# Kernel optimization log

Measured on AMD Instinct MI355X. Metric: run time of the kernel, lower is better.

The kernel has to match this reference:

```python
import jax, jax.numpy as jnp
import numpy as np
from jax import lax

B, NE, ZD, GAMMA, BETA = 16384, 512, 32, 0.99, 1.0

def conv2d(x, w, b, stride, pad):
    y = lax.conv_general_dilated(x, w, (stride, stride), [(pad, pad), (pad, pad)],
                                 dimension_numbers=('NCHW', 'OIHW', 'NCHW'))
    return y if b is None else y + b[None, :, None, None]

def convt2d(x, w, b, stride, pad):
    # torch ConvTranspose2d(w: [in,out,kh,kw]) == dilated conv with flipped, transposed kernel
    k = w.shape[2]
    wf = jnp.flip(w, (2, 3)).transpose(1, 0, 2, 3)  # -> [out,in,kh,kw]
    p = k - 1 - pad
    y = lax.conv_general_dilated(x, wf, (1, 1), [(p, p), (p, p)], lhs_dilation=(stride, stride),
                                 dimension_numbers=('NCHW', 'OIHW', 'NCHW'))
    return y + b[None, :, None, None]

def res_stack(x, w1, w2):
    # ResidualLayer: relu -> conv3x3 (32->64) -> relu -> conv1x1 (64->32), add; stack ends with relu
    r = jax.nn.relu(x)
    r = conv2d(r, w1, None, 1, 1)
    r = jax.nn.relu(r)
    r = conv2d(r, w2, None, 1, 0)
    return jax.nn.relu(x + r)

def linear(x, w, b):
    return x @ w.T + b

def setup_inputs() -> dict:
    key = jax.random.key(0)
    ks = jax.random.split(key, 24)
    g = lambda k, s, sc=0.05: (jax.random.normal(k, s) * sc).astype(jnp.float32)
    inp = {
        'x': jax.random.uniform(ks[0], (B, 1, 28, 28), dtype=jnp.float32),
        'conv1_w': g(ks[1], (16, 1, 4, 4)), 'conv1_b': jnp.zeros((16,), jnp.float32),
        'conv2_w': g(ks[2], (32, 16, 4, 4)), 'conv2_b': jnp.zeros((32,), jnp.float32),
        'res1_w1': g(ks[3], (64, 32, 3, 3)), 'res1_w2': g(ks[4], (32, 64, 1, 1)),
        'fc1_w': g(ks[5], (224, 1568)), 'fc1_b': jnp.zeros((224,), jnp.float32),
        'fc2_w': g(ks[6], (ZD, 224)), 'fc2_b': jnp.zeros((ZD,), jnp.float32),
        'emb': jax.random.uniform(ks[7], (NE, ZD), jnp.float32, -1.0 / NE, 1.0 / NE),
        'n_mat': jnp.ones((NE,), jnp.float32),
        'm_mat': jnp.ones((NE, ZD), jnp.float32),
        'fc3_w': g(ks[8], (224, ZD)), 'fc3_b': jnp.zeros((224,), jnp.float32),
        'fc4_w': g(ks[9], (1568, 224)), 'fc4_b': jnp.zeros((1568,), jnp.float32),
        'res2_w1': g(ks[10], (64, 32, 3, 3)), 'res2_w2': g(ks[11], (32, 64, 1, 1)),
        'convt1_w': g(ks[12], (32, 16, 4, 4)), 'convt1_b': jnp.zeros((16,), jnp.float32),
        'convt2_w': g(ks[13], (16, 1, 4, 4)), 'convt2_b': jnp.zeros((1,), jnp.float32),
    }
    return inp

def vq(z, emb, n_mat, m_mat):
    # z: [N, ZD]; nearest-codeword assignment
    d = (jnp.sum(z * z, 1, keepdims=True) + jnp.sum(emb * emb, 1)
         - 2.0 * (z @ emb.T))                                   # [N, NE]
    idx = jnp.argmin(d, axis=1)                                  # [N]
    z_q = jnp.take(emb, idx, axis=0)                             # [N, ZD]
    counts = jax.ops.segment_sum(jnp.ones((z.shape[0],), z.dtype), idx, num_segments=NE)
    sums = jax.ops.segment_sum(lax.stop_gradient(z), idx, num_segments=NE)
    n_new = n_mat * GAMMA + counts * (1.0 - GAMMA)
    m_new = m_mat * GAMMA + sums * (1.0 - GAMMA)
    emb_new = m_new / n_new[:, None]
    commit_loss = BETA * jnp.mean((lax.stop_gradient(z_q) - z) ** 2)
    quant_loss = jnp.mean((z_q - lax.stop_gradient(z)) ** 2)
    z_q_st = z + lax.stop_gradient(z_q - z)                      # straight-through
    e_mean = counts / z.shape[0]
    perplexity = jnp.exp(-jnp.sum(e_mean * jnp.log(e_mean + 1e-10)))
    return quant_loss, commit_loss, z_q_st, perplexity, emb_new

def reference(x, conv1_w, conv1_b, conv2_w, conv2_b, res1_w1, res1_w2,
              fc1_w, fc1_b, fc2_w, fc2_b, emb, n_mat, m_mat,
              fc3_w, fc3_b, fc4_w, fc4_b, res2_w1, res2_w2,
              convt1_w, convt1_b, convt2_w, convt2_b):
    # encoder: 28x28 -> 14x14 -> 7x7
    h = jax.nn.relu(conv2d(x, conv1_w, conv1_b, 2, 1))
    h = conv2d(h, conv2_w, conv2_b, 2, 1)
    h = res_stack(h, res1_w1, res1_w2)
    h = h.reshape(h.shape[0], -1)                                # [B, 1568]
    h = jax.nn.relu(linear(h, fc1_w, fc1_b))
    z = linear(h, fc2_w, fc2_b)                                  # [B, ZD]
    quant_loss, commit_loss, z_q, perplexity, emb_new = vq(z, emb, n_mat, m_mat)
    # decoder
    h = jax.nn.relu(linear(z_q, fc3_w, fc3_b))
    h = jax.nn.relu(linear(h, fc4_w, fc4_b))
    h = h.reshape(-1, 32, 7, 7)
    h = res_stack(h, res2_w1, res2_w2)
    h = jax.nn.relu(convt2d(h, convt1_w, convt1_b, 2, 1))
    x_rec = convt2d(h, convt2_w, convt2_b, 2, 1)                 # [B,1,28,28]
    return x_rec, quant_loss, commit_loss, perplexity, emb_new
```

## Files before the change

### kernel.cpp

```cpp
#include <hip/hip_runtime.h>
#include <math.h>

#define NB 16384
typedef unsigned short ushort_t;
typedef unsigned int uint_t;
typedef __attribute__((ext_vector_type(8))) short short8;
typedef __attribute__((ext_vector_type(4))) float fx4;

static const size_t OFF_HB    = 0;
static const size_t OFF_F1B   = 12845056;
static const size_t OFF_F3B   = 14680064;
static const size_t OFF_Z     = 16515072;
static const size_t OFF_IDX   = 17039360;
static const size_t OFF_ZQB   = 17055744;
static const size_t OFF_CNT   = 17317888;
static const size_t OFF_SUM   = 17318400;
static const size_t OFF_LOSS  = 17334784;
static const size_t OFF_WENC  = 17334848;
static const size_t OFF_WT1B  = 17343040;
static const size_t OFF_WR1B  = 17351232;
static const size_t OFF_WR2B  = 17360448;
static const size_t OFF_W2B1  = 17369664;
static const size_t OFF_W2B2  = 17370688;
static const size_t OFF_FC1WB = 17371712;
static const size_t OFF_FC2WB = 17547328;
static const size_t OFF_FC3WB = 17550912;
static const size_t OFF_FC4WB = 17554496;

static __device__ __forceinline__ ushort_t f2bf(float f) {
  union { float f; uint_t u; } v; v.f = f;
  return (ushort_t)((v.u + 0x7fffu + ((v.u >> 16) & 1u)) >> 16);
}
static __device__ __forceinline__ float bf2f(ushort_t h) {
  union { uint_t u; float f; } v; v.u = ((uint_t)h) << 16;
  return v.f;
}

__global__ __launch_bounds__(256) void k_prep(
    const float* __restrict__ c2w, const float* __restrict__ r1w1,
    const float* __restrict__ r1w2, const float* __restrict__ r2w1,
    const float* __restrict__ r2w2, const float* __restrict__ t1w,
    const float* __restrict__ fc1w, const float* __restrict__ fc2w,
    const float* __restrict__ fc3w, const float* __restrict__ fc4w,
    float* __restrict__ ws)
{
  int gid = blockIdx.x * 256 + threadIdx.x;
  if (gid == 0) ws[OFF_LOSS] = 0.f;
  if (gid >= 774144) return;
  ushort_t* wencb = (ushort_t*)(ws + OFF_WENC);
  ushort_t* wt1b  = (ushort_t*)(ws + OFF_WT1B);
  ushort_t* wr1b  = (ushort_t*)(ws + OFF_WR1B);
  ushort_t* wr2b  = (ushort_t*)(ws + OFF_WR2B);
  ushort_t* w2b1  = (ushort_t*)(ws + OFF_W2B1);
  ushort_t* w2b2  = (ushort_t*)(ws + OFF_W2B2);
  ushort_t* fc1wb = (ushort_t*)(ws + OFF_FC1WB);
  ushort_t* fc2wb = (ushort_t*)(ws + OFF_FC2WB);
  ushort_t* fc3wb = (ushort_t*)(ws + OFF_FC3WB);
  ushort_t* fc4wb = (ushort_t*)(ws + OFF_FC4WB);
  int i = gid;
  if (i < 8192) {
    int kidx = i & 31, rest = i >> 5, co = rest & 31, kb = rest >> 5;
    int ky = kb >> 1, k2 = kb & 1, kxs = kidx >> 4, ci = kidx & 15;
    wencb[i] = f2bf(c2w[co*256 + ci*16 + ky*4 + 2*k2 + kxs]);
  } else if (i < 16384) {
    int j = i - 8192, ci = j & 31, rest = j >> 5, co = rest & 15, kk = rest >> 4;
    wt1b[j] = f2bf(t1w[ci*256 + co*16 + kk]);
  } else if (i < 34816) {
    int j = i - 16384, ci = j & 31, r = j >> 5, co = r & 63, kk = r >> 6;
    wr1b[j] = f2bf(r1w1[co*288 + ci*9 + kk]);
  } else if (i < 53248) {
    int j = i - 34816, ci = j & 31, r = j >> 5, co = r & 63, kk = r >> 6;
    wr2b[j] = f2bf(r2w1[co*288 + ci*9 + kk]);
  } else if (i < 55296) {
    int j = i - 53248; w2b1[j] = f2bf(r1w2[j]);
  } else if (i < 57344) {
    int j = i - 55296; w2b2[j] = f2bf(r2w2[j]);
  } else if (i < 408576) {
    int j = i - 57344; fc1wb[j] = f2bf(fc1w[j]);
  } else if (i < 415744) {
    int j = i - 408576; fc2wb[j] = f2bf(fc2w[j]);
  } else if (i < 422912) {
    int j = i - 415744; fc3wb[j] = f2bf(fc3w[j]);
  } else {
    int j = i - 422912; fc4wb[j] = f2bf(fc4w[j]);
  }
}

__global__ __launch_bounds__(256) void k_enc(const float* __restrict__ x,
    const float* __restrict__ w1, const float* __restrict__ b1,
    const ushort_t* __restrict__ wencb, const float* __restrict__ b2,
    ushort_t* __restrict__ hb)
{
  __shared__ float xin[30][32];
  __shared__ ushort_t ph1b[256*24];
  __shared__ ushort_t outl[1568];
  int b = blockIdx.x, t = threadIdx.x, l = t & 63, w = t >> 6;
  int pr = l & 15, g = l >> 4;
  short8 bf[8][2];
  #pragma unroll
  for (int kb = 0; kb < 8; ++kb)
    #pragma unroll
    for (int nt = 0; nt < 2; ++nt)
      bf[kb][nt] = *(const short8*)(wencb + (size_t)(kb*32 + nt*16 + pr)*32 + g*8);
  uint_t* pz = (uint_t*)ph1b;
  for (int i = t; i < 3072; i += 256) pz[i] = 0;
  float* xp = &xin[0][0];
  for (int i = t; i < 960; i += 256) xp[i] = 0.f;
  __syncthreads();
  const float* xb = x + (size_t)b*784;
  for (int i = t; i < 784; i += 256) xin[i/28 + 1][i%28 + 1] = xb[i];
  __syncthreads();
  char* phc = (char*)ph1b;
  for (int i = t; i < 3136; i += 256) {
    int p = i >> 4, co = i & 15, oy = p/14, ox = p%14;
    float acc = b1[co];
    #pragma unroll
    for (int ky = 0; ky < 4; ++ky)
      #pragma unroll
      for (int kx = 0; kx < 4; ++kx)
        acc += xin[2*oy+ky][2*ox+kx] * w1[co*16 + ky*4 + kx];
    int prow = (oy+1)*16 + (ox+1);
    *(ushort_t*)(phc + prow*48 + co*2) = f2bf(fmaxf(acc, 0.f));
  }
  __syncthreads();
  int p = w*16 + pr; if (p > 48) p = 48;
  int oy = p/7, ox = p%7;
  fx4 acc2[2];
  acc2[0] = (fx4){0.f,0.f,0.f,0.f}; acc2[1] = (fx4){0.f,0.f,0.f,0.f};
  #pragma unroll
  for (int kb = 0; kb < 8; ++kb) {
    int ky = kb >> 1, k2 = kb & 1;
    int prow = (2*oy + ky)*16 + 2*ox + 2*k2 + (g >> 1);
    short8 afr = *(const short8*)(phc + prow*48 + (g & 1)*16);
    acc2[0] = __builtin_amdgcn_mfma_f32_16x16x32_bf16(afr, bf[kb][0], acc2[0], 0, 0, 0);
    acc2[1] = __builtin_amdgcn_mfma_f32_16x16x32_bf16(afr, bf[kb][1], acc2[1], 0, 0, 0);
  }
  #pragma unroll
  for (int nt = 0; nt < 2; ++nt) {
    int co = nt*16 + pr;
    float bv = b2[co];
    #pragma unroll
    for (int i = 0; i < 4; ++i) {
      int pix = w*16 + g*4 + i;
      if (pix < 49) outl[co*49 + pix] = f2bf(acc2[nt][i] + bv);
    }
  }
  __syncthreads();
  uint_t* dst = (uint_t*)(hb + (size_t)b*1568);
  const uint_t* so = (const uint_t*)outl;
  for (int j = t; j < 784; j += 256) dst[j] = so[j];
}

__global__ __launch_bounds__(256) void k_res(ushort_t* __restrict__ hb,
    const ushort_t* __restrict__ wrb, const ushort_t* __restrict__ w2b)
{
  __shared__ ushort_t pinT[3456];
  __shared__ ushort_t rl[4096];
  __shared__ ushort_t hrawb[1568];
  __shared__ ushort_t outl[1568];
  int b = blockIdx.x, t = threadIdx.x, l = t & 63, w = t >> 6, g = l >> 4;

  short8 bfr[9];
  #pragma unroll
  for (int o = 0; o < 9; ++o)
    bfr[o] = *(const short8*)(wrb + (size_t)(o*64 + w*16 + (l & 15))*32 + g*8);

  uint_t* pz = (uint_t*)pinT;
  for (int i = t; i < 1728; i += 256) pz[i] = 0;
  __syncthreads();

  const uint_t* src = (const uint_t*)(hb + (size_t)b*1568);
  char* pinc = (char*)pinT;
  for (int j = t; j < 784; j += 256) {
    uint_t u = src[j];
    ((uint_t*)hrawb)[j] = u;
    #pragma unroll
    for (int h = 0; h < 2; ++h) {
      int i = 2*j + h;
      ushort_t us = (ushort_t)(h ? (u >> 16) : (u & 0xffff));
      ushort_t ur = (us & 0x8000) ? (ushort_t)0 : us;
      int ci = i / 49, p = i % 49, y = p / 7, xx = p % 7;
      int ppix = (y + 1)*12 + (xx + 1);
      int byte = ((ppix << 6) + (ci << 1)) ^ ((ppix & 6) << 3);
      *(ushort_t*)(pinc + byte) = ur;
    }
  }
  __syncthreads();

  fx4 acc[4];
  #pragma unroll
  for (int mt = 0; mt < 4; ++mt) acc[mt] = (fx4){0.f, 0.f, 0.f, 0.f};
  int pb[4];
  #pragma unroll
  for (int mt = 0; mt < 4; ++mt) {
    int p = mt*16 + (l & 15); if (p > 48) p = 48;
    pb[mt] = (p / 7)*12 + (p % 7);
  }
  #pragma unroll
  for (int mt = 0; mt < 4; ++mt) {
    #pragma unroll
    for (int o = 0; o < 9; ++o) {
      int ppix = pb[mt] + (o / 3)*12 + (o % 3);
      int byte = ((ppix << 6) + (g << 4)) ^ ((ppix & 6) << 3);
      short8 afr = *(const short8*)(pinc + byte);
      acc[mt] = __builtin_amdgcn_mfma_f32_16x16x32_bf16(afr, bfr[o], acc[mt], 0, 0, 0);
    }
  }
  char* rlc = (char*)rl;
  #pragma unroll
  for (int mt = 0; mt < 4; ++mt) {
    #pragma unroll
    for (int i = 0; i < 4; ++i) {
      int pixr = mt*16 + g*4 + i;
      int co2 = w*16 + (l & 15);
      int byte = ((pixr << 7) + (co2 << 1)) ^ ((pixr & 7) << 4);
      *(ushort_t*)(rlc + byte) = f2bf(fmaxf(acc[mt][i], 0.f));
    }
  }
  __syncthreads();

  fx4 a1[2];
  a1[0] = (fx4){0.f,0.f,0.f,0.f}; a1[1] = (fx4){0.f,0.f,0.f,0.f};
  int prr = w*16 + (l & 15);
  #pragma unroll
  for (int kf = 0; kf < 2; ++kf) {
    int byte = ((prr << 7) + (kf << 6) + (g << 4)) ^ ((prr & 7) << 4);
    short8 ar = *(const short8*)(rlc + byte);
    #pragma unroll
    for (int nt = 0; nt < 2; ++nt) {
      short8 br = *(const short8*)(w2b + (size_t)(nt*16 + (l & 15))*64 + kf*32 + g*8);
      a1[nt] = __builtin_amdgcn_mfma_f32_16x16x32_bf16(ar, br, a1[nt], 0, 0, 0);
    }
  }
  #pragma unroll
  for (int nt = 0; nt < 2; ++nt) {
    #pragma unroll
    for (int i = 0; i < 4; ++i) {
      int pix = w*16 + g*4 + i;
      if (pix < 49) {
        int co2 = nt*16 + (l & 15);
        int idx2 = co2*49 + pix;
        float v = bf2f(hrawb[idx2]) + a1[nt][i];
        outl[idx2] = f2bf(fmaxf(v, 0.f));
      }
    }
  }
  __syncthreads();
  uint_t* dst = (uint_t*)(hb + (size_t)b*1568);
  const uint_t* so = (const uint_t*)outl;
  for (int j = t; j < 784; j += 256) dst[j] = so[j];
}

template<int BNF, bool OUTBF16, bool RELU>
__global__ __launch_bounds__(256) void k_mm(const ushort_t* __restrict__ A,
    const ushort_t* __restrict__ Wb, const float* __restrict__ bias,
    void* __restrict__ C, int M, int N, int K)
{
  __shared__ ushort_t As[2048];
  int t = threadIdx.x, l = t & 63, w = t >> 6, g = l >> 4;
  int m0 = blockIdx.x * 64, n0 = blockIdx.y * (BNF * 16);
  fx4 acc[BNF];
  #pragma unroll
  for (int nt = 0; nt < BNF; ++nt) acc[nt] = (fx4){0.f, 0.f, 0.f, 0.f};
  char* asc = (char*)As;
  int srow = t >> 2, sks = (t & 3) * 8;
  int sbyte = ((srow << 6) + (sks << 1)) ^ ((srow & 6) << 3);
  int arow = w*16 + (l & 15);
  int abyte = ((arow << 6) + (g << 4)) ^ ((arow & 6) << 3);
  for (int k0 = 0; k0 < K; k0 += 32) {
    short8 av = *(const short8*)(A + (size_t)(m0 + srow)*K + k0 + sks);
    __syncthreads();
    *(short8*)(asc + sbyte) = av;
    __syncthreads();
    short8 afr = *(const short8*)(asc + abyte);
    #pragma unroll
    for (int nt = 0; nt < BNF; ++nt) {
      short8 bfr = *(const short8*)(Wb + (size_t)(n0 + nt*16 + (l & 15))*K + k0 + g*8);
      acc[nt] = __builtin_amdgcn_mfma_f32_16x16x32_bf16(afr, bfr, acc[nt], 0, 0, 0);
    }
  }
  #pragma unroll
  for (int nt = 0; nt < BNF; ++nt) {
    int col = n0 + nt*16 + (l & 15);
    float bv = bias[col];
    #pragma unroll
    for (int i = 0; i < 4; ++i) {
      int row = m0 + w*16 + g*4 + i;
      float v = acc[nt][i] + bv;
      if (RELU) v = fmaxf(v, 0.f);
      if (OUTBF16) ((ushort_t*)C)[(size_t)row*N + col] = f2bf(v);
      else         ((float*)C)[(size_t)row*N + col] = v;
    }
  }
}

__global__ __launch_bounds__(256) void k_vq_assign(const float* __restrict__ z,
    const float* __restrict__ emb, ushort_t* __restrict__ zqb, int* __restrict__ idx,
    float* __restrict__ loss)
{
  __shared__ float esq[512];
  int t = threadIdx.x;
  int n = blockIdx.x * 256 + t;
  for (int e = t; e < 512; e += 256) {
    const float4* ep = (const float4*)&emb[e*32];
    float s = 0.f;
    #pragma unroll
    for (int q = 0; q < 8; ++q) { float4 v = ep[q]; s += v.x*v.x + v.y*v.y + v.z*v.z + v.w*v.w; }
    esq[e] = s;
  }
  __syncthreads();
  float zv[32];
  const float4* zp = (const float4*)&z[n*32];
  float zz = 0.f;
  #pragma unroll
  for (int q = 0; q < 8; ++q) {
    float4 v = zp[q];
    zv[4*q]=v.x; zv[4*q+1]=v.y; zv[4*q+2]=v.z; zv[4*q+3]=v.w;
    zz += v.x*v.x + v.y*v.y + v.z*v.z + v.w*v.w;
  }
  float best = 3.4e38f; int bi = 0;
  for (int e = 0; e < 512; ++e) {
    const float4* ep = (const float4*)&emb[e*32];
    float dot = 0.f;
    #pragma unroll
    for (int q = 0; q < 8; ++q) {
      float4 v = ep[q];
      dot += zv[4*q]*v.x + zv[4*q+1]*v.y + zv[4*q+2]*v.z + zv[4*q+3]*v.w;
    }
    float d = zz + esq[e] - 2.f*dot;
    if (d < best) { best = d; bi = e; }
  }
  idx[n] = bi;
  const float4* bp = (const float4*)&emb[bi*32];
  uint_t* zo = (uint_t*)(zqb + (size_t)n*32);
  float ls = 0.f;
  #pragma unroll
  for (int q = 0; q < 8; ++q) {
    float4 v = bp[q];
    zo[q*2]   = (uint_t)f2bf(v.x) | ((uint_t)f2bf(v.y) << 16);
    zo[q*2+1] = (uint_t)f2bf(v.z) | ((uint_t)f2bf(v.w) << 16);
    float d0 = v.x - zv[4*q], d1 = v.y - zv[4*q+1];
    float d2 = v.z - zv[4*q+2], d3 = v.w - zv[4*q+3];
    ls += d0*d0 + d1*d1 + d2*d2 + d3*d3;
  }
  #pragma unroll
  for (int m = 32; m >= 1; m >>= 1) ls += __shfl_xor(ls, m);
  if ((t & 63) == 0) atomicAdd(loss, ls);
}

__global__ __launch_bounds__(64) void k_vq_reduce(const int* __restrict__ idx,
    const float* __restrict__ z, float* __restrict__ counts, float* __restrict__ sums)
{
  int e = blockIdx.x, t = threadIdx.x;
  float cnt = 0.f, sv[32];
  #pragma unroll
  for (int k = 0; k < 32; ++k) sv[k] = 0.f;
  for (int n = t; n < 16384; n += 64) {
    if (idx[n] == e) {
      cnt += 1.f;
      const float4* zp = (const float4*)&z[n*32];
      #pragma unroll
      for (int q = 0; q < 8; ++q) {
        float4 v = zp[q];
        sv[4*q] += v.x; sv[4*q+1] += v.y; sv[4*q+2] += v.z; sv[4*q+3] += v.w;
      }
    }
  }
  #pragma unroll
  for (int m = 32; m >= 1; m >>= 1) {
    cnt += __shfl_xor(cnt, m);
    #pragma unroll
    for (int k = 0; k < 32; ++k) sv[k] += __shfl_xor(sv[k], m);
  }
  if (t == 0) {
    counts[e] = cnt;
    #pragma unroll
    for (int k = 0; k < 32; ++k) sums[e*32 + k] = sv[k];
  }
}

__global__ __launch_bounds__(512) void k_vq_final(const float* __restrict__ counts,
    const float* __restrict__ sums, const float* __restrict__ n_mat,
    const float* __restrict__ m_mat, const float* __restrict__ loss,
    float* __restrict__ out)
{
  __shared__ float red[8];
  int t = threadIdx.x;
  float c = counts[t];
  float nn = n_mat[t]*0.99f + c*0.01f;
  #pragma unroll
  for (int k = 0; k < 32; ++k) {
    float mn = m_mat[t*32+k]*0.99f + sums[t*32+k]*0.01f;
    out[12845059 + t*32 + k] = mn / nn;
  }
  float em = c * (1.f/16384.f);
  float ht = em * logf(em + 1e-10f);
  #pragma unroll
  for (int m = 32; m >= 1; m >>= 1) ht += __shfl_xor(ht, m);
  if ((t & 63) == 0) red[t >> 6] = ht;
  __syncthreads();
  if (t == 0) {
    float H = 0.f;
    #pragma unroll
    for (int i = 0; i < 8; ++i) H += red[i];
    float q = loss[0] * (1.f/524288.f);
    out[12845056] = q;
    out[12845057] = q;
    out[12845058] = expf(-H);
  }
}

__global__ __launch_bounds__(256) void k_dec(const ushort_t* __restrict__ h5,
    const ushort_t* __restrict__ wt1b, const float* __restrict__ bt1,
    const float* __restrict__ wt2, const float* __restrict__ bt2,
    float* __restrict__ out)
{
  __shared__ ushort_t pinT[3456];
  __shared__ ushort_t pt1b[256*20];
  __shared__ float w2l[256];
  __shared__ float outl[784];
  int b = blockIdx.x, t = threadIdx.x, l = t & 63, w = t >> 6;
  int pr = l & 15, g = l >> 4;
  int py = w >> 1, px = w & 1;
  short8 bfr[4];
  #pragma unroll
  for (int r = 0; r < 2; ++r)
    #pragma unroll
    for (int c = 0; c < 2; ++c) {
      int kk = (3 - py - 2*r)*4 + (3 - px - 2*c);
      bfr[r*2 + c] = *(const short8*)(wt1b + (size_t)(kk*16 + pr)*32 + g*8);
    }
  uint_t* pz = (uint_t*)pinT;
  for (int i = t; i < 1728; i += 256) pz[i] = 0;
  uint_t* qz = (uint_t*)pt1b;
  for (int i = t; i < 2560; i += 256) qz[i] = 0;
  if (t < 256) w2l[t] = wt2[t];
  __syncthreads();
  const uint_t* src = (const uint_t*)(h5 + (size_t)b*1568);
  char* pinc = (char*)pinT;
  for (int j = t; j < 784; j += 256) {
    uint_t u = src[j];
    #pragma unroll
    for (int h = 0; h < 2; ++h) {
      int i = 2*j + h;
      ushort_t us = (ushort_t)(h ? (u >> 16) : (u & 0xffff));
      int ci = i / 49, p = i % 49, y = p / 7, xx = p % 7;
      int ppix = (y + 1)*12 + (xx + 1);
      int byte = ((ppix << 6) + (ci << 1)) ^ ((ppix & 6) << 3);
      *(ushort_t*)(pinc + byte) = us;
    }
  }
  __syncthreads();
  fx4 acc[4];
  #pragma unroll
  for (int mt = 0; mt < 4; ++mt) acc[mt] = (fx4){0.f, 0.f, 0.f, 0.f};
  int pb[4];
  #pragma unroll
  for (int mt = 0; mt < 4; ++mt) {
    int p = mt*16 + pr; if (p > 48) p = 48;
    pb[mt] = (p / 7)*12 + (p % 7);
  }
  #pragma unroll
  for (int mt = 0; mt < 4; ++mt) {
    #pragma unroll
    for (int r = 0; r < 2; ++r)
      #pragma unroll
      for (int c = 0; c < 2; ++c) {
        int ppix = pb[mt] + (py + r)*12 + (px + c);
        int byte = ((ppix << 6) + (g << 4)) ^ ((ppix & 6) << 3);
        short8 afr = *(const short8*)(pinc + byte);
        acc[mt] = __builtin_amdgcn_mfma_f32_16x16x32_bf16(afr, bfr[r*2 + c], acc[mt], 0, 0, 0);
      }
  }
  char* ptc = (char*)pt1b;
  float bv1 = bt1[pr];
  #pragma unroll
  for (int mt = 0; mt < 4; ++mt) {
    #pragma unroll
    for (int i = 0; i < 4; ++i) {
      int p = mt*16 + g*4 + i;
      if (p < 49) {
        int yy = p / 7, xx = p % 7;
        int opix = (2*yy + py + 1)*16 + (2*xx + px + 1);
        *(ushort_t*)(ptc + opix*40 + pr*2) = f2bf(fmaxf(acc[mt][i] + bv1, 0.f));
      }
    }
  }
  __syncthreads();
  {
    int qy = w >> 1, qx = w & 1;
    float wreg[4][16];
    int kkt[4] = { qy*4 + qx, qy*4 + qx + 2, (qy+2)*4 + qx, (qy+2)*4 + qx + 2 };
    #pragma unroll
    for (int tt = 0; tt < 4; ++tt)
      #pragma unroll
      for (int ci = 0; ci < 16; ++ci)
        wreg[tt][ci] = w2l[ci*16 + kkt[tt]];
    float bv2 = bt2[0];
    #pragma unroll
    for (int k = 0; k < 4; ++k) {
      int j = l + k*64;
      if (j < 196) {
        int a = j / 14, bb = j % 14;
        int oy = 2*a + 1 - qy, ox = 2*bb + 1 - qx;
        int iy1 = a + 1 - qy, iy2 = a - qy;
        int ix1 = bb + 1 - qx, ix2 = bb - qx;
        int prw[4];
        prw[0] = (iy1 + 1)*16 + (ix1 + 1);
        prw[1] = (iy1 + 1)*16 + (ix2 + 1);
        prw[2] = (iy2 + 1)*16 + (ix1 + 1);
        prw[3] = (iy2 + 1)*16 + (ix2 + 1);
        float s = bv2;
        #pragma unroll
        for (int tt = 0; tt < 4; ++tt) {
          #pragma unroll
          for (int jj = 0; jj < 4; ++jj) {
            uint2 v = *(const uint2*)(ptc + prw[tt]*40 + jj*8);
            s += bf2f((ushort_t)(v.x & 0xffff)) * wreg[tt][jj*4+0]
               + bf2f((ushort_t)(v.x >> 16))    * wreg[tt][jj*4+1]
               + bf2f((ushort_t)(v.y & 0xffff)) * wreg[tt][jj*4+2]
               + bf2f((ushort_t)(v.y >> 16))    * wreg[tt][jj*4+3];
          }
        }
        outl[oy*28 + ox] = s;
      }
    }
  }
  __syncthreads();
  float* dst = out + (size_t)b*784;
  for (int i = t; i < 784; i += 256) dst[i] = outl[i];
}

extern "C" void kernel_launch(void* const* d_in, const int* in_sizes, int n_in,
                              void* d_out, int out_size, void* d_ws, size_t ws_size,
                              hipStream_t stream)
{
  const float* x    = (const float*)d_in[0];
  const float* c1w  = (const float*)d_in[1];
  const float* c1b  = (const float*)d_in[2];
  const float* c2w  = (const float*)d_in[3];
  const float* c2b  = (const float*)d_in[4];
  const float* r1w1 = (const float*)d_in[5];
  const float* r1w2 = (const float*)d_in[6];
  const float* fc1w = (const float*)d_in[7];
  const float* fc1b = (const float*)d_in[8];
  const float* fc2w = (const float*)d_in[9];
  const float* fc2b = (const float*)d_in[10];
  const float* emb  = (const float*)d_in[11];
  const float* nmat = (const float*)d_in[12];
  const float* mmat = (const float*)d_in[13];
  const float* fc3w = (const float*)d_in[14];
  const float* fc3b = (const float*)d_in[15];
  const float* fc4w = (const float*)d_in[16];
  const float* fc4b = (const float*)d_in[17];
  const float* r2w1 = (const float*)d_in[18];
  const float* r2w2 = (const float*)d_in[19];
  const float* t1w  = (const float*)d_in[20];
  const float* t1b  = (const float*)d_in[21];
  const float* t2w  = (const float*)d_in[22];
  const float* t2b  = (const float*)d_in[23];
  float* ws  = (float*)d_ws;
  float* out = (float*)d_out;

  ushort_t* hb   = (ushort_t*)(ws + OFF_HB);
  ushort_t* f1b  = (ushort_t*)(ws + OFF_F1B);
  ushort_t* f3b  = (ushort_t*)(ws + OFF_F3B);
  float*    z    = ws + OFF_Z;
  int*      idx  = (int*)(ws + OFF_IDX);
  ushort_t* zqb  = (ushort_t*)(ws + OFF_ZQB);
  float*    cnts = ws + OFF_CNT;
  float*    sums = ws + OFF_SUM;
  float*    loss = ws + OFF_LOSS;
  ushort_t* wencb = (ushort_t*)(ws + OFF_WENC);
  ushort_t* wt1b  = (ushort_t*)(ws + OFF_WT1B);
  ushort_t* wr1b  = (ushort_t*)(ws + OFF_WR1B);
  ushort_t* wr2b  = (ushort_t*)(ws + OFF_WR2B);
  ushort_t* w2b1  = (ushort_t*)(ws + OFF_W2B1);
  ushort_t* w2b2  = (ushort_t*)(ws + OFF_W2B2);
  ushort_t* fc1wb = (ushort_t*)(ws + OFF_FC1WB);
  ushort_t* fc2wb = (ushort_t*)(ws + OFF_FC2WB);
  ushort_t* fc3wb = (ushort_t*)(ws + OFF_FC3WB);
  ushort_t* fc4wb = (ushort_t*)(ws + OFF_FC4WB);

  k_prep<<<3024, 256, 0, stream>>>(c2w, r1w1, r1w2, r2w1, r2w2, t1w,
                                   fc1w, fc2w, fc3w, fc4w, ws);
  k_enc<<<NB, 256, 0, stream>>>(x, c1w, c1b, wencb, c2b, hb);
  k_res<<<NB, 256, 0, stream>>>(hb, wr1b, w2b1);
  k_mm<14, true, true><<<dim3(256, 1), 256, 0, stream>>>(hb, fc1wb, fc1b, f1b, 16384, 224, 1568);
  k_mm<2, false, false><<<dim3(256, 1), 256, 0, stream>>>(f1b, fc2wb, fc2b, z, 16384, 32, 224);
  k_vq_assign<<<64, 256, 0, stream>>>(z, emb, zqb, idx, loss);
  k_vq_reduce<<<512, 64, 0, stream>>>(idx, z, cnts, sums);
  k_vq_final<<<1, 512, 0, stream>>>(cnts, sums, nmat, mmat, loss, out);
  k_mm<14, true, true><<<dim3(256, 1), 256, 0, stream>>>(zqb, fc3wb, fc3b, f3b, 16384, 224, 32);
  k_mm<14, true, true><<<dim3(256, 7), 256, 0, stream>>>(f3b, fc4wb, fc4b, hb, 16384, 1568, 224);
  k_res<<<NB, 256, 0, stream>>>(hb, wr2b, w2b2);
  k_dec<<<NB, 256, 0, stream>>>(hb, wt1b, t1b, t2w, t2b, out);
}
```

Before: 987.0 us.

## Switch intermediate activations to channel-last layout, fp16 dot2 decoder, prefetch in GEMM

```diff
diff --git a/kernel.cpp b/kernel.cpp
--- a/kernel.cpp
+++ b/kernel.cpp
@@ -6,6 +6,8 @@
 typedef unsigned int uint_t;
 typedef __attribute__((ext_vector_type(8))) short short8;
 typedef __attribute__((ext_vector_type(4))) float fx4;
+typedef _Float16 half2v __attribute__((ext_vector_type(2)));
+typedef _Float16 half4v __attribute__((ext_vector_type(4)));
 
 static const size_t OFF_HB    = 0;
 static const size_t OFF_F1B   = 12845056;
@@ -26,6 +28,7 @@
 static const size_t OFF_FC2WB = 17547328;
 static const size_t OFF_FC3WB = 17550912;
 static const size_t OFF_FC4WB = 17554496;
+static const size_t OFF_FC4BP = 17730112;
 
 static __device__ __forceinline__ ushort_t f2bf(float f) {
   union { float f; uint_t u; } v; v.f = f;
@@ -34,6 +37,13 @@
 static __device__ __forceinline__ float bf2f(ushort_t h) {
   union { uint_t u; float f; } v; v.u = ((uint_t)h) << 16;
   return v.f;
+}
+static __device__ __forceinline__ float fdot2(half2v a, half2v b, float c) {
+#if __has_builtin(__builtin_amdgcn_fdot2)
+  return __builtin_amdgcn_fdot2(a, b, c, false);
+#else
+  return c + (float)a.x * (float)b.x + (float)a.y * (float)b.y;
+#endif
 }
 
 __global__ __launch_bounds__(256) void k_prep(
@@ -42,11 +52,11 @@
     const float* __restrict__ r2w2, const float* __restrict__ t1w,
     const float* __restrict__ fc1w, const float* __restrict__ fc2w,
     const float* __restrict__ fc3w, const float* __restrict__ fc4w,
-    float* __restrict__ ws)
+    const float* __restrict__ fc4b, float* __restrict__ ws)
 {
   int gid = blockIdx.x * 256 + threadIdx.x;
   if (gid == 0) ws[OFF_LOSS] = 0.f;
-  if (gid >= 774144) return;
+  if (gid >= 775712) return;
   ushort_t* wencb = (ushort_t*)(ws + OFF_WENC);
   ushort_t* wt1b  = (ushort_t*)(ws + OFF_WT1B);
   ushort_t* wr1b  = (ushort_t*)(ws + OFF_WR1B);
@@ -57,6 +67,7 @@
   ushort_t* fc2wb = (ushort_t*)(ws + OFF_FC2WB);
   ushort_t* fc3wb = (ushort_t*)(ws + OFF_FC3WB);
   ushort_t* fc4wb = (ushort_t*)(ws + OFF_FC4WB);
+  float*    fc4bp = ws + OFF_FC4BP;
   int i = gid;
   if (i < 8192) {
     int kidx = i & 31, rest = i >> 5, co = rest & 31, kb = rest >> 5;
@@ -76,13 +87,20 @@
   } else if (i < 57344) {
     int j = i - 55296; w2b2[j] = f2bf(r2w2[j]);
   } else if (i < 408576) {
-    int j = i - 57344; fc1wb[j] = f2bf(fc1w[j]);
+    int j = i - 57344, n = j / 1568, k = j % 1568;
+    int p = k >> 5, ci = k & 31;
+    fc1wb[j] = f2bf(fc1w[n*1568 + ci*49 + p]);
   } else if (i < 415744) {
     int j = i - 408576; fc2wb[j] = f2bf(fc2w[j]);
   } else if (i < 422912) {
     int j = i - 415744; fc3wb[j] = f2bf(fc3w[j]);
+  } else if (i < 774144) {
+    int j = i - 422912, np = j / 224, k = j % 224;
+    int p = np >> 5, ci = np & 31;
+    fc4wb[j] = f2bf(fc4w[(ci*49 + p)*224 + k]);
   } else {
-    int j = i - 422912; fc4wb[j] = f2bf(fc4w[j]);
+    int np = i - 774144, p = np >> 5, ci = np & 31;
+    fc4bp[np] = fc4b[ci*49 + p];
   }
 }
 
@@ -96,6 +114,11 @@
   __shared__ ushort_t outl[1568];
   int b = blockIdx.x, t = threadIdx.x, l = t & 63, w = t >> 6;
   int pr = l & 15, g = l >> 4;
+  int co16 = t & 15;
+  float wr1v[16];
+  #pragma unroll
+  for (int kk = 0; kk < 16; ++kk) wr1v[kk] = w1[co16*16 + kk];
+  float bv1 = b1[co16];
   short8 bf[8][2];
   #pragma unroll
   for (int kb = 0; kb < 8; ++kb)
@@ -112,15 +135,14 @@
   __syncthreads();
   char* phc = (char*)ph1b;
   for (int i = t; i < 3136; i += 256) {
-    int p = i >> 4, co = i & 15, oy = p/14, ox = p%14;
-    float acc = b1[co];
+    int p = i >> 4, oy = p/14, ox = p%14;
+    float acc = bv1;
     #pragma unroll
     for (int ky = 0; ky < 4; ++ky)
       #pragma unroll
       for (int kx = 0; kx < 4; ++kx)
-        acc += xin[2*oy+ky][2*ox+kx] * w1[co*16 + ky*4 + kx];
-    int prow = (oy+1)*16 + (ox+1);
-    *(ushort_t*)(phc + prow*48 + co*2) = f2bf(fmaxf(acc, 0.f));
+        acc += xin[2*oy+ky][2*ox+kx] * wr1v[ky*4+kx];
+    *(ushort_t*)(phc + ((oy+1)*16 + (ox+1))*48 + co16*2) = f2bf(fmaxf(acc, 0.f));
   }
   __syncthreads();
   int p = w*16 + pr; if (p > 48) p = 48;
@@ -142,7 +164,7 @@
     #pragma unroll
     for (int i = 0; i < 4; ++i) {
       int pix = w*16 + g*4 + i;
-      if (pix < 49) outl[co*49 + pix] = f2bf(acc2[nt][i] + bv);
+      if (pix < 49) outl[pix*32 + co] = f2bf(acc2[nt][i] + bv);
     }
   }
   __syncthreads();
@@ -174,16 +196,13 @@
   for (int j = t; j < 784; j += 256) {
     uint_t u = src[j];
     ((uint_t*)hrawb)[j] = u;
-    #pragma unroll
-    for (int h = 0; h < 2; ++h) {
-      int i = 2*j + h;
-      ushort_t us = (ushort_t)(h ? (u >> 16) : (u & 0xffff));
-      ushort_t ur = (us & 0x8000) ? (ushort_t)0 : us;
-      int ci = i / 49, p = i % 49, y = p / 7, xx = p % 7;
-      int ppix = (y + 1)*12 + (xx + 1);
-      int byte = ((ppix << 6) + (ci << 1)) ^ ((ppix & 6) << 3);
-      *(ushort_t*)(pinc + byte) = ur;
-    }
+    uint_t ur = u;
+    ur = (ur & 0x80000000u) ? (ur & 0x0000ffffu) : ur;
+    ur = (ur & 0x8000u)     ? (ur & 0xffff0000u) : ur;
+    int p = j >> 4, c2 = (j & 15) << 1;
+    int ppix = (p/7 + 1)*12 + (p%7) + 1;
+    int byte = ((ppix << 6) + (c2 << 1)) ^ ((ppix & 6) << 3);
+    *(uint_t*)(pinc + byte) = ur;
   }
   __syncthreads();
 
@@ -239,7 +258,7 @@
       int pix = w*16 + g*4 + i;
       if (pix < 49) {
         int co2 = nt*16 + (l & 15);
-        int idx2 = co2*49 + pix;
+        int idx2 = pix*32 + co2;
         float v = bf2f(hrawb[idx2]) + a1[nt][i];
         outl[idx2] = f2bf(fmaxf(v, 0.f));
       }
@@ -267,11 +286,13 @@
   int sbyte = ((srow << 6) + (sks << 1)) ^ ((srow & 6) << 3);
   int arow = w*16 + (l & 15);
   int abyte = ((arow << 6) + (g << 4)) ^ ((arow & 6) << 3);
+  const ushort_t* ap = A + (size_t)(m0 + srow)*K + sks;
+  short8 av = *(const short8*)ap;
   for (int k0 = 0; k0 < K; k0 += 32) {
-    short8 av = *(const short8*)(A + (size_t)(m0 + srow)*K + k0 + sks);
     __syncthreads();
     *(short8*)(asc + sbyte) = av;
     __syncthreads();
+    if (k0 + 32 < K) av = *(const short8*)(ap + k0 + 32);
     short8 afr = *(const short8*)(asc + abyte);
     #pragma unroll
     for (int nt = 0; nt < BNF; ++nt) {
@@ -440,15 +461,10 @@
   char* pinc = (char*)pinT;
   for (int j = t; j < 784; j += 256) {
     uint_t u = src[j];
-    #pragma unroll
-    for (int h = 0; h < 2; ++h) {
-      int i = 2*j + h;
-      ushort_t us = (ushort_t)(h ? (u >> 16) : (u & 0xffff));
-      int ci = i / 49, p = i % 49, y = p / 7, xx = p % 7;
-      int ppix = (y + 1)*12 + (xx + 1);
-      int byte = ((ppix << 6) + (ci << 1)) ^ ((ppix & 6) << 3);
-      *(ushort_t*)(pinc + byte) = us;
-    }
+    int p = j >> 4, c2 = (j & 15) << 1;
+    int ppix = (p/7 + 1)*12 + (p%7) + 1;
+    int byte = ((ppix << 6) + (c2 << 1)) ^ ((ppix & 6) << 3);
+    *(uint_t*)(pinc + byte) = u;
   }
   __syncthreads();
   fx4 acc[4];
@@ -482,20 +498,22 @@
       if (p < 49) {
         int yy = p / 7, xx = p % 7;
         int opix = (2*yy + py + 1)*16 + (2*xx + px + 1);
-        *(ushort_t*)(ptc + opix*40 + pr*2) = f2bf(fmaxf(acc[mt][i] + bv1, 0.f));
+        *(_Float16*)(ptc + opix*40 + pr*2) = (_Float16)(fmaxf(acc[mt][i] + bv1, 0.f));
       }
     }
   }
   __syncthreads();
   {
     int qy = w >> 1, qx = w & 1;
-    float wreg[4][16];
     int kkt[4] = { qy*4 + qx, qy*4 + qx + 2, (qy+2)*4 + qx, (qy+2)*4 + qx + 2 };
+    half2v wh[4][8];
     #pragma unroll
     for (int tt = 0; tt < 4; ++tt)
       #pragma unroll
-      for (int ci = 0; ci < 16; ++ci)
-        wreg[tt][ci] = w2l[ci*16 + kkt[tt]];
+      for (int q = 0; q < 8; ++q) {
+        wh[tt][q].x = (_Float16)w2l[(2*q)*16 + kkt[tt]];
+        wh[tt][q].y = (_Float16)w2l[(2*q+1)*16 + kkt[tt]];
+      }
     float bv2 = bt2[0];
     #pragma unroll
     for (int k = 0; k < 4; ++k) {
@@ -513,13 +531,17 @@
         float s = bv2;
         #pragma unroll
         for (int tt = 0; tt < 4; ++tt) {
+          const char* base = ptc + prw[tt]*40;
           #pragma unroll
-          for (int jj = 0; jj < 4; ++jj) {
-            uint2 v = *(const uint2*)(ptc + prw[tt]*40 + jj*8);
-            s += bf2f((ushort_t)(v.x & 0xffff)) * wreg[tt][jj*4+0]
-               + bf2f((ushort_t)(v.x >> 16))    * wreg[tt][jj*4+1]
-               + bf2f((ushort_t)(v.y & 0xffff)) * wreg[tt][jj*4+2]
-               + bf2f((ushort_t)(v.y >> 16))    * wreg[tt][jj*4+3];
+          for (int jj = 0; jj < 2; ++jj) {
+            half4v a4 = *(const half4v*)(base + jj*8);
+            half4v b4 = *(const half4v*)(base + 16 + jj*8);
+            half2v a0 = {a4.x, a4.y}, a1 = {a4.z, a4.w};
+            half2v b0 = {b4.x, b4.y}, b1 = {b4.z, b4.w};
+            s = fdot2(a0, wh[tt][jj*2],     s);
+            s = fdot2(a1, wh[tt][jj*2 + 1], s);
+            s = fdot2(b0, wh[tt][jj*2 + 4], s);
+            s = fdot2(b1, wh[tt][jj*2 + 5], s);
           }
         }
         outl[oy*28 + ox] = s;
@@ -581,9 +603,10 @@
   ushort_t* fc2wb = (ushort_t*)(ws + OFF_FC2WB);
   ushort_t* fc3wb = (ushort_t*)(ws + OFF_FC3WB);
   ushort_t* fc4wb = (ushort_t*)(ws + OFF_FC4WB);
-
-  k_prep<<<3024, 256, 0, stream>>>(c2w, r1w1, r1w2, r2w1, r2w2, t1w,
-                                   fc1w, fc2w, fc3w, fc4w, ws);
+  float*    fc4bp = ws + OFF_FC4BP;
+
+  k_prep<<<3031, 256, 0, stream>>>(c2w, r1w1, r1w2, r2w1, r2w2, t1w,
+                                   fc1w, fc2w, fc3w, fc4w, fc4b, ws);
   k_enc<<<NB, 256, 0, stream>>>(x, c1w, c1b, wencb, c2b, hb);
   k_res<<<NB, 256, 0, stream>>>(hb, wr1b, w2b1);
   k_mm<14, true, true><<<dim3(256, 1), 256, 0, stream>>>(hb, fc1wb, fc1b, f1b, 16384, 224, 1568);
@@ -592,7 +615,7 @@
   k_vq_reduce<<<512, 64, 0, stream>>>(idx, z, cnts, sums);
   k_vq_final<<<1, 512, 0, stream>>>(cnts, sums, nmat, mmat, loss, out);
   k_mm<14, true, true><<<dim3(256, 1), 256, 0, stream>>>(zqb, fc3wb, fc3b, f3b, 16384, 224, 32);
-  k_mm<14, true, true><<<dim3(256, 7), 256, 0, stream>>>(f3b, fc4wb, fc4b, hb, 16384, 1568, 224);
+  k_mm<14, true, true><<<dim3(256, 7), 256, 0, stream>>>(f3b, fc4wb, fc4bp, hb, 16384, 1568, 224);
   k_res<<<NB, 256, 0, stream>>>(hb, wr2b, w2b2);
   k_dec<<<NB, 256, 0, stream>>>(hb, wt1b, t1b, t2w, t2b, out);
 }
```

Result: no change. 994.3 us (+0.7%).
